# Kernel tuning notes

Hardware: AMD Instinct MI355X
Metric: run time of the kernel (lower is better)

Reference implementation:

```python
import jax, jax.numpy as jnp
import numpy as np

B, L, H = 16, 4096, 768

def setup_inputs() -> dict:
    key = jax.random.key(0)
    k1, k2 = jax.random.split(key)
    sequence_output = jax.random.normal(k1, (B, L, H), dtype=jnp.float32)
    # sorted segment ids: each wordpiece position maps to a token index in [0, L)
    wordpiece_to_token = jnp.sort(
        jax.random.randint(k2, (B, L), 0, L, dtype=jnp.int32), axis=-1)
    return {"sequence_output": sequence_output,
            "wordpiece_to_token": wordpiece_to_token}

def reference(sequence_output, wordpiece_to_token):
    # For each (batch, token j): output[b, j] = sum of sequence_output[b, p]
    # over wordpieces p assigned to token j. Tokens with no wordpieces stay 0,
    # matching torch.zeros_like initialization in the original.
    num_tokens = sequence_output.shape[1]
    def per_example(x, seg):  # x: [L, H], seg: [L]
        return jax.ops.segment_sum(x, seg, num_segments=num_tokens)
    return jax.vmap(per_example)(sequence_output, wordpiece_to_token)
```

## Files before the change

### kernel.cpp

```cpp
#include <hip/hip_runtime.h>

#define BB 16
#define LL 4096
#define H4 192

__global__ __launch_bounds__(256) void segsum_fused_kernel(
    const float4* __restrict__ x, const int* __restrict__ seg,
    float4* __restrict__ out) {
    int gtid = blockIdx.x * blockDim.x + threadIdx.x;
    int wave = gtid >> 6;
    int lane = gtid & 63;
    int b = wave >> 12;
    int j = wave & (LL - 1);

    const int* __restrict__ sb = seg + ((size_t)b << 12);

    int v1 = sb[lane << 6];
    unsigned long long ms = __ballot(v1 >= j);
    unsigned long long me = __ballot(v1 > j);

    int s, e;
    if (ms & 1ull) {
        s = 0;
    } else {
        int f = ms ? (__ffsll((unsigned long long)ms) - 1) : 64;
        int base = ((f - 1) << 6) + 1;
        int p2 = base + lane;
        int v2 = (p2 < LL) ? sb[p2] : 0x7fffffff;
        unsigned long long m2 = __ballot(v2 >= j);
        s = base + __ffsll(m2) - 1;
    }
    if (me & 1ull) {
        e = 0;
    } else {
        int f = me ? (__ffsll((unsigned long long)me) - 1) : 64;
        int base = ((f - 1) << 6) + 1;
        int p2 = base + lane;
        int v2 = (p2 < LL) ? sb[p2] : 0x7fffffff;
        unsigned long long m2 = __ballot(v2 > j);
        e = base + __ffsll(m2) - 1;
    }

    float4 a0 = make_float4(0.f, 0.f, 0.f, 0.f);
    float4 a1 = a0, a2 = a0;

    const float4* xb = x + (size_t)b * LL * H4;
    for (int p = s; p < e; ++p) {
        const float4* row = xb + (size_t)p * H4 + lane;
        float4 v0 = row[0];
        float4 vA = row[64];
        float4 vB = row[128];
        a0.x += v0.x; a0.y += v0.y; a0.z += v0.z; a0.w += v0.w;
        a1.x += vA.x; a1.y += vA.y; a1.z += vA.z; a1.w += vA.w;
        a2.x += vB.x; a2.y += vB.y; a2.z += vB.z; a2.w += vB.w;
    }

    float4* orow = out + (size_t)wave * H4 + lane;
    orow[0]   = a0;
    orow[64]  = a1;
    orow[128] = a2;
}

extern "C" void kernel_launch(void* const* d_in, const int* in_sizes, int n_in,
                              void* d_out, int out_size, void* d_ws, size_t ws_size,
                              hipStream_t stream) {
    const float* x   = (const float*)d_in[0];
    const int*   seg = (const int*)d_in[1];
    float* out = (float*)d_out;
    (void)d_ws; (void)ws_size;

    int nblocks = (BB * LL) / 4;
    segsum_fused_kernel<<<nblocks, 256, 0, stream>>>(
        (const float4*)x, seg, (float4*)out);
}
```

Baseline: 328.9 us.

## Process four consecutive tokens per wave with a software-pipelined segment walk

Each wave now handles four adjacent output tokens. It does one pair of binary searches for the combined wordpiece range, then walks that range once, writing out accumulators whenever the segment id advances. This cuts the number of segment searches fourfold. It also prefetches the next row and its segment id one iteration ahead to overlap load latency. In exchange there are fewer waves and less parallelism, plus extra branching and a data-dependent inner flush loop.

```diff
diff --git a/kernel.cpp b/kernel.cpp
--- a/kernel.cpp
+++ b/kernel.cpp
@@ -3,62 +3,86 @@
 #define BB 16
 #define LL 4096
 #define H4 192
+#define TPW 4
 
-__global__ __launch_bounds__(256) void segsum_fused_kernel(
+__global__ __launch_bounds__(256) void segsum_kernel(
     const float4* __restrict__ x, const int* __restrict__ seg,
     float4* __restrict__ out) {
     int gtid = blockIdx.x * blockDim.x + threadIdx.x;
     int wave = gtid >> 6;
     int lane = gtid & 63;
-    int b = wave >> 12;
-    int j = wave & (LL - 1);
+    int b  = wave >> 10;
+    int j0 = (wave & 1023) << 2;
 
     const int* __restrict__ sb = seg + ((size_t)b << 12);
 
     int v1 = sb[lane << 6];
-    unsigned long long ms = __ballot(v1 >= j);
-    unsigned long long me = __ballot(v1 > j);
+    unsigned long long ms = __ballot(v1 >= j0);
+    unsigned long long me = __ballot(v1 >= (j0 + TPW));
 
     int s, e;
     if (ms & 1ull) {
         s = 0;
     } else {
-        int f = ms ? (__ffsll((unsigned long long)ms) - 1) : 64;
+        int f = ms ? (__ffsll(ms) - 1) : 64;
         int base = ((f - 1) << 6) + 1;
         int p2 = base + lane;
         int v2 = (p2 < LL) ? sb[p2] : 0x7fffffff;
-        unsigned long long m2 = __ballot(v2 >= j);
+        unsigned long long m2 = __ballot(v2 >= j0);
         s = base + __ffsll(m2) - 1;
     }
     if (me & 1ull) {
         e = 0;
     } else {
-        int f = me ? (__ffsll((unsigned long long)me) - 1) : 64;
+        int f = me ? (__ffsll(me) - 1) : 64;
         int base = ((f - 1) << 6) + 1;
         int p2 = base + lane;
         int v2 = (p2 < LL) ? sb[p2] : 0x7fffffff;
-        unsigned long long m2 = __ballot(v2 > j);
+        unsigned long long m2 = __ballot(v2 >= (j0 + TPW));
         e = base + __ffsll(m2) - 1;
     }
 
-    float4 a0 = make_float4(0.f, 0.f, 0.f, 0.f);
-    float4 a1 = a0, a2 = a0;
+    const float4* xb = x + (size_t)b * LL * H4;
+    float4* ob = out + (((size_t)b << 12) + j0) * H4 + lane;
 
-    const float4* xb = x + (size_t)b * LL * H4;
-    for (int p = s; p < e; ++p) {
+    float4 a0 = make_float4(0.f, 0.f, 0.f, 0.f), a1 = a0, a2 = a0;
+    int d = 0;
+
+    float4 b0 = a0, b1 = a0, b2 = a0;
+    int sp = 0;
+    int p = s;
+    if (p < e) {
         const float4* row = xb + (size_t)p * H4 + lane;
-        float4 v0 = row[0];
-        float4 vA = row[64];
-        float4 vB = row[128];
-        a0.x += v0.x; a0.y += v0.y; a0.z += v0.z; a0.w += v0.w;
-        a1.x += vA.x; a1.y += vA.y; a1.z += vA.z; a1.w += vA.w;
-        a2.x += vB.x; a2.y += vB.y; a2.z += vB.z; a2.w += vB.w;
+        b0 = row[0]; b1 = row[64]; b2 = row[128];
+        sp = sb[p];
     }
-
-    float4* orow = out + (size_t)wave * H4 + lane;
-    orow[0]   = a0;
-    orow[64]  = a1;
-    orow[128] = a2;
+    while (p < e) {
+        int pn = p + 1;
+        float4 c0 = a0, c1 = a0, c2 = a0;
+        int spn = 0;
+        if (pn < e) {
+            const float4* row = xb + (size_t)pn * H4 + lane;
+            c0 = row[0]; c1 = row[64]; c2 = row[128];
+            spn = sb[pn];
+        }
+        while (j0 + d < sp) {
+            float4* orow = ob + (size_t)d * H4;
+            orow[0] = a0; orow[64] = a1; orow[128] = a2;
+            a0 = make_float4(0.f, 0.f, 0.f, 0.f); a1 = a0; a2 = a0;
+            ++d;
+        }
+        a0.x += b0.x; a0.y += b0.y; a0.z += b0.z; a0.w += b0.w;
+        a1.x += b1.x; a1.y += b1.y; a1.z += b1.z; a1.w += b1.w;
+        a2.x += b2.x; a2.y += b2.y; a2.z += b2.z; a2.w += b2.w;
+        b0 = c0; b1 = c1; b2 = c2; sp = spn;
+        p = pn;
+    }
+    while (d < TPW) {
+        float4* orow = ob + (size_t)d * H4;
+        orow[0] = a0; orow[64] = a1; orow[128] = a2;
+        a0 = make_float4(0.f, 0.f, 0.f, 0.f); a1 = a0; a2 = a0;
+        ++d;
+    }
 }
 
 extern "C" void kernel_launch(void* const* d_in, const int* in_sizes, int n_in,
@@ -69,7 +93,7 @@
     float* out = (float*)d_out;
     (void)d_ws; (void)ws_size;
 
-    int nblocks = (BB * LL) / 4;
-    segsum_fused_kernel<<<nblocks, 256, 0, stream>>>(
+    int nblocks = (BB * LL / TPW) / 4;
+    segsum_kernel<<<nblocks, 256, 0, stream>>>(
         (const float4*)x, seg, (float4*)out);
 }
```

After: 339.9 us. 1.03x slower.
